# Performance work log

Hardware: AMD Instinct MI355X
Metric: run time of the kernel (lower is better)

## Reference

```python
import jax, jax.numpy as jnp
import numpy as np

H = 1024          # hidden_dim
N_AVAIL = 32768   # number of available ops (rows of the score matrix)
N_M = 64          # machines
N_OP = 40000      # unfinished ops
N_JOB = 2000      # jobs
L = 4             # policy_num_layers


def setup_inputs() -> dict:
    key = jax.random.key(0)
    ks = jax.random.split(key, 12)
    s_in = (2.0 / (2 * H + 2)) ** 0.5   # kaiming-ish scale
    s_h = (2.0 / H) ** 0.5
    return {
        "x_m": jax.random.normal(ks[0], (N_M, H), jnp.float32),
        "x_op": jax.random.normal(ks[1], (N_OP, H), jnp.float32),
        "job_srpt": jax.random.uniform(ks[2], (N_JOB,), jnp.float32),
        "pt": jax.random.uniform(ks[3], (N_AVAIL,), jnp.float32),  # process_time / max_process_time
        "W0": jax.random.normal(ks[4], (2 * H + 2, H), jnp.float32) * s_in,
        "b0": jnp.zeros((H,), jnp.float32),
        "W1": jax.random.normal(ks[5], (H, H), jnp.float32) * s_h,
        "b1": jnp.zeros((H,), jnp.float32),
        "W2": jax.random.normal(ks[6], (H, H), jnp.float32) * s_h,
        "b2": jnp.zeros((H,), jnp.float32),
        "W3": jax.random.normal(ks[7], (H, 1), jnp.float32) * s_h,
        "b3": jnp.zeros((1,), jnp.float32),
        "m_ids": jax.random.randint(ks[8], (N_AVAIL,), 0, N_M, jnp.int32),
        "op_idx": jax.random.randint(ks[9], (N_AVAIL,), 0, N_OP, jnp.int32),
        "job_ids": jax.random.randint(ks[10], (N_AVAIL,), 0, N_JOB, jnp.int32),
    }


def reference(x_m, x_op, job_srpt, pt, W0, b0, W1, b1, W2, b2, W3, b3,
              m_ids, op_idx, job_ids):
    # Batched gather + concat: replaces the per-op Python loop of torch.cat's.
    feat = jnp.concatenate(
        [x_m[m_ids],                     # [N, H]
         x_op[op_idx],                   # [N, H]
         job_srpt[job_ids][:, None],     # [N, 1]
         pt[:, None]],                   # [N, 1]
        axis=1)                          # [N, 2H+2]
    lrelu = lambda v: jax.nn.leaky_relu(v, 0.01)
    h = lrelu(feat @ W0 + b0)
    h = lrelu(h @ W1 + b1)
    h = lrelu(h @ W2 + b2)
    score = (h @ W3 + b3).ravel()        # [N]
    probs = jax.nn.softmax(score)        # softmax over available ops (dim=0)
    idx = jnp.argmax(score)              # greedy action
    return probs, idx
```

## Files before the change

kernel.cpp:

```cpp
#include <hip/hip_runtime.h>
#include <hip/hip_bf16.h>

typedef __attribute__((ext_vector_type(8))) short short8;
typedef __attribute__((ext_vector_type(4))) float f32x4;

#define GL2LDS16(g, l)                                                         \
  __builtin_amdgcn_global_load_lds(                                            \
      (const __attribute__((address_space(1))) unsigned int*)(g),              \
      (__attribute__((address_space(3))) unsigned int*)(l), 16, 0, 0)

__device__ __forceinline__ short8 lds_read_b128(const __hip_bfloat16* p) {
  short8 v;
  asm volatile("ds_read_b128 %0, %1"
               : "=v"(v)
               : "v"((unsigned)(uintptr_t)p));
  return v;
}

__global__ __launch_bounds__(256) void feat_kernel(
    const float* __restrict__ x_m, const float* __restrict__ x_op,
    const float* __restrict__ job_srpt, const int* __restrict__ m_ids,
    const int* __restrict__ op_idx, const int* __restrict__ job_ids,
    __hip_bfloat16* __restrict__ feat, float* __restrict__ srow) {
  const int row = blockIdx.x;
  const int t = threadIdx.x;
  const int j0 = t * 8;
  const float* src;
  if (j0 < 1024)
    src = x_m + (long)m_ids[row] * 1024 + j0;
  else
    src = x_op + (long)op_idx[row] * 1024 + (j0 - 1024);
  float4 v0 = *(const float4*)src;
  float4 v1 = *(const float4*)(src + 4);
  union {
    __hip_bfloat16 h[8];
    int4 i4;
  } u;
  u.h[0] = __float2bfloat16(v0.x);
  u.h[1] = __float2bfloat16(v0.y);
  u.h[2] = __float2bfloat16(v0.z);
  u.h[3] = __float2bfloat16(v0.w);
  u.h[4] = __float2bfloat16(v1.x);
  u.h[5] = __float2bfloat16(v1.y);
  u.h[6] = __float2bfloat16(v1.z);
  u.h[7] = __float2bfloat16(v1.w);
  *(int4*)&feat[(long)row * 2048 + j0] = u.i4;
  if (t == 0) srow[row] = job_srpt[job_ids[row]];
}

__global__ __launch_bounds__(256) void wconv_kernel(
    const float* __restrict__ W, __hip_bfloat16* __restrict__ Wt, int K) {
  __shared__ float tile[64][65];
  const int kb = blockIdx.x * 64;
  const int nb = blockIdx.y * 64;
  const int t = threadIdx.x;
#pragma unroll
  for (int it = 0; it < 16; ++it) {
    int idx = it * 256 + t;
    int kk = idx >> 6, nn = idx & 63;
    tile[kk][nn] = W[(long)(kb + kk) * 1024 + nb + nn];
  }
  __syncthreads();
#pragma unroll
  for (int it = 0; it < 16; ++it) {
    int idx = it * 256 + t;
    int nn = idx >> 6, kk = idx & 63;
    Wt[(long)(nb + nn) * K + kb + kk] = __float2bfloat16(tile[kk][nn]);
  }
}

__global__ __launch_bounds__(512, 2) void gemm_kernel(
    const __hip_bfloat16* __restrict__ A, const __hip_bfloat16* __restrict__ Bt,
    __hip_bfloat16* __restrict__ C, const float* __restrict__ bias, int M,
    int N, int K, int rank2, const float* __restrict__ wr0,
    const float* __restrict__ wr1, const float* __restrict__ srow,
    const float* __restrict__ ptv, int fuseW3,
    const float* __restrict__ W3, float* __restrict__ scoreOut) {
  __shared__ __align__(16) __hip_bfloat16 As[2][256 * 64];
  __shared__ __align__(16) __hip_bfloat16 Bs[2][256 * 64];
  const int t = threadIdx.x;
  const int lane = t & 63;
  const int wid = t >> 6;
  const int wm = wid >> 2;
  const int wn = wid & 3;
  const long arow0 = (long)blockIdx.x * 256;
  const int bcol0 = blockIdx.y * 256;
  const int NT = K >> 6;

  const int sa_row = ((t >> 8) * 128) + ((t >> 3) & 31);
  const int sb_row = t >> 3;
  const int scol = ((t & 7) ^ ((t >> 3) & 7)) * 8;

#define STAGE_A(buf, kt1, p)                                                   \
  GL2LDS16(A + (arow0 + sa_row + (p) * 32) * (long)K + (kt1) * 64 + scol,      \
           &As[buf][(t >> 8) * 8192 + (p) * 2048 + (t & 255) * 8])
#define STAGE_B(buf, kt1, q)                                                   \
  GL2LDS16(Bt + (long)(bcol0 + sb_row + (q) * 64) * (long)K + (kt1) * 64 + scol, \
           &Bs[buf][(q) * 4096 + t * 8])

  f32x4 acc[8][4] = {};
  short8 bfr[8];

#pragma unroll
  for (int q = 0; q < 4; ++q) STAGE_B(0, 0, q);
#pragma unroll
  for (int p = 0; p < 4; ++p) STAGE_A(0, 0, p);

  for (int kt = 0; kt < NT; ++kt) {
    const int cur = kt & 1;
    const bool pre = (kt + 1) < NT;
#pragma unroll
    for (int p = 0; p < 4; ++p) {
      if (pre) {
        if (p == 0) { STAGE_B(cur ^ 1, kt + 1, 0); STAGE_B(cur ^ 1, kt + 1, 1); }
        if (p == 1) { STAGE_B(cur ^ 1, kt + 1, 2); STAGE_B(cur ^ 1, kt + 1, 3); }
        if (p == 2) { STAGE_A(cur ^ 1, kt + 1, 0); STAGE_A(cur ^ 1, kt + 1, 1); }
        if (p == 3) { STAGE_A(cur ^ 1, kt + 1, 2); STAGE_A(cur ^ 1, kt + 1, 3); }
        asm volatile("s_waitcnt vmcnt(4)" ::: "memory");
      } else {
        asm volatile("s_waitcnt vmcnt(0)" ::: "memory");
      }
      __builtin_amdgcn_s_barrier();

      short8 af[2][2];
      if (p == 0) {
#pragma unroll
        for (int j = 0; j < 4; ++j)
#pragma unroll
          for (int ks = 0; ks < 2; ++ks) {
            const int ko = (ks * 32 + ((lane >> 4) << 3)) ^ ((lane & 7) << 3);
            bfr[j * 2 + ks] =
                lds_read_b128(&Bs[cur][(wn * 64 + j * 16 + (lane & 15)) * 64 + ko]);
          }
      }
#pragma unroll
      for (int ii = 0; ii < 2; ++ii)
#pragma unroll
        for (int ks = 0; ks < 2; ++ks) {
          const int ko = (ks * 32 + ((lane >> 4) << 3)) ^ ((lane & 7) << 3);
          af[ii][ks] = lds_read_b128(
              &As[cur][(wm * 128 + (2 * p + ii) * 16 + (lane & 15)) * 64 + ko]);
        }

      asm volatile("s_waitcnt lgkmcnt(0)" ::: "memory");
      __builtin_amdgcn_sched_barrier(0);
      __builtin_amdgcn_s_setprio(1);
#pragma unroll
      for (int ii = 0; ii < 2; ++ii)
#pragma unroll
        for (int ks = 0; ks < 2; ++ks)
#pragma unroll
          for (int j = 0; j < 4; ++j)
            acc[2 * p + ii][j] = __builtin_amdgcn_mfma_f32_16x16x32_bf16(
                af[ii][ks], bfr[j * 2 + ks], acc[2 * p + ii][j], 0, 0, 0);
      __builtin_amdgcn_s_setprio(0);
      __builtin_amdgcn_s_barrier();
    }
  }

  if (!fuseW3) {
#pragma unroll
    for (int j = 0; j < 4; ++j) {
      const int c = bcol0 + wn * 64 + j * 16 + (lane & 15);
      const float bia = bias[c];
      float wa = 0.f, wb = 0.f;
      if (rank2) {
        wa = wr0[c];
        wb = wr1[c];
      }
#pragma unroll
      for (int i = 0; i < 8; ++i) {
        const long rb = arow0 + wm * 128 + i * 16 + ((lane >> 4) << 2);
#pragma unroll
        for (int g = 0; g < 4; ++g) {
          const long r = rb + g;
          float v = acc[i][j][g] + bia;
          if (rank2) v += srow[r] * wa + ptv[r] * wb;
          v = v > 0.f ? v : 0.01f * v;
          C[r * N + c] = __float2bfloat16(v);
        }
      }
    }
  } else {
    float bia[4], w3v[4];
#pragma unroll
    for (int j = 0; j < 4; ++j) {
      const int c = bcol0 + wn * 64 + j * 16 + (lane & 15);
      bia[j] = bias[c];
      w3v[j] = W3[c];
    }
#pragma unroll
    for (int i = 0; i < 8; ++i) {
#pragma unroll
      for (int g = 0; g < 4; ++g) {
        float ps = 0.f;
#pragma unroll
        for (int j = 0; j < 4; ++j) {
          float v = acc[i][j][g] + bia[j];
          v = v > 0.f ? v : 0.01f * v;
          ps += v * w3v[j];
        }
        ps += __shfl_xor(ps, 1);
        ps += __shfl_xor(ps, 2);
        ps += __shfl_xor(ps, 4);
        ps += __shfl_xor(ps, 8);
        if ((lane & 15) == 0) {
          const long r = arow0 + wm * 128 + i * 16 + ((lane >> 4) << 2) + g;
          atomicAdd(&scoreOut[r], ps);
        }
      }
    }
  }
#undef STAGE_A
#undef STAGE_B
}

__global__ __launch_bounds__(256) void redmax_kernel(
    const float* __restrict__ score, float* __restrict__ pmax,
    int* __restrict__ pidx) {
  const int t = threadIdx.x, b = blockIdx.x;
  float m = -1e30f;
  int mi = 0;
#pragma unroll
  for (int u = 0; u < 2; ++u) {
    int i = b * 512 + u * 256 + t;
    float v = score[i];
    if (v > m) {
      m = v;
      mi = i;
    }
  }
  __shared__ float sm[4];
  __shared__ int si[4];
#pragma unroll
  for (int off = 32; off; off >>= 1) {
    float om = __shfl_down(m, off);
    int oi = __shfl_down(mi, off);
    if (om > m || (om == m && oi < mi)) {
      m = om;
      mi = oi;
    }
  }
  const int lane = t & 63, w = t >> 6;
  if (lane == 0) {
    sm[w] = m;
    si[w] = mi;
  }
  __syncthreads();
  if (t == 0) {
    for (int w2 = 1; w2 < 4; ++w2)
      if (sm[w2] > m || (sm[w2] == m && si[w2] < mi)) {
        m = sm[w2];
        mi = si[w2];
      }
    pmax[b] = m;
    pidx[b] = mi;
  }
}

__global__ __launch_bounds__(64) void finmax_kernel(
    const float* __restrict__ pmax, const int* __restrict__ pidx,
    float* __restrict__ gscal, float* __restrict__ out_idx) {
  const int t = threadIdx.x;
  float m = pmax[t];
  int mi = pidx[t];
#pragma unroll
  for (int off = 32; off; off >>= 1) {
    float om = __shfl_down(m, off);
    int oi = __shfl_down(mi, off);
    if (om > m || (om == m && oi < mi)) {
      m = om;
      mi = oi;
    }
  }
  if (t == 0) {
    gscal[0] = m;
    out_idx[0] = (float)mi;
  }
}

__global__ __launch_bounds__(256) void expsum_kernel(
    const float* __restrict__ score, const float* __restrict__ gscal,
    float* __restrict__ e, float* __restrict__ psum) {
  const int t = threadIdx.x, b = blockIdx.x;
  const float gmax = gscal[0];
  float s = 0.f;
#pragma unroll
  for (int u = 0; u < 2; ++u) {
    int i = b * 512 + u * 256 + t;
    float v = expf(score[i] - gmax);
    e[i] = v;
    s += v;
  }
#pragma unroll
  for (int off = 32; off; off >>= 1) s += __shfl_down(s, off);
  __shared__ float sm[4];
  const int lane = t & 63, w = t >> 6;
  if (lane == 0) sm[w] = s;
  __syncthreads();
  if (t == 0) psum[b] = sm[0] + sm[1] + sm[2] + sm[3];
}

__global__ __launch_bounds__(64) void finsum_kernel(const float* __restrict__ psum,
                                                    float* __restrict__ gscal) {
  float s = psum[threadIdx.x];
#pragma unroll
  for (int off = 32; off; off >>= 1) s += __shfl_down(s, off);
  if (threadIdx.x == 0) gscal[1] = 1.0f / s;
}

__global__ __launch_bounds__(256) void scale_kernel(float* __restrict__ e,
                                                    const float* __restrict__ gscal) {
  const float inv = gscal[1];
  const int i = blockIdx.x * 512 + threadIdx.x;
  e[i] *= inv;
  e[i + 256] *= inv;
}

extern "C" void kernel_launch(void* const* d_in, const int* in_sizes, int n_in,
                              void* d_out, int out_size, void* d_ws,
                              size_t ws_size, hipStream_t stream) {
  const float* x_m = (const float*)d_in[0];
  const float* x_op = (const float*)d_in[1];
  const float* job_srpt = (const float*)d_in[2];
  const float* pt = (const float*)d_in[3];
  const float* W0 = (const float*)d_in[4];
  const float* b0 = (const float*)d_in[5];
  const float* W1 = (const float*)d_in[6];
  const float* b1 = (const float*)d_in[7];
  const float* W2 = (const float*)d_in[8];
  const float* b2 = (const float*)d_in[9];
  const float* W3 = (const float*)d_in[10];
  const int* m_ids = (const int*)d_in[12];
  const int* op_idx = (const int*)d_in[13];
  const int* job_ids = (const int*)d_in[14];

  const int M = 32768;

  char* p = (char*)d_ws;
  __hip_bfloat16* feat = (__hip_bfloat16*)p;            p += (size_t)M * 2048 * 2;
  __hip_bfloat16* hA = (__hip_bfloat16*)p;              p += (size_t)M * 1024 * 2;
  __hip_bfloat16* hB = (__hip_bfloat16*)p;              p += (size_t)M * 1024 * 2;
  __hip_bfloat16* Wt0 = (__hip_bfloat16*)p;             p += (size_t)1024 * 2048 * 2;
  __hip_bfloat16* Wt1 = (__hip_bfloat16*)p;             p += (size_t)1024 * 1024 * 2;
  __hip_bfloat16* Wt2 = (__hip_bfloat16*)p;             p += (size_t)1024 * 1024 * 2;
  float* srow = (float*)p;                              p += (size_t)M * 4;
  float* score = (float*)p;                             p += (size_t)M * 4;
  float* pmax = (float*)p;                              p += 256;
  int* pidx = (int*)p;                                  p += 256;
  float* psum = (float*)p;                              p += 256;
  float* gscal = (float*)p;                             p += 256;

  float* probs = (float*)d_out;
  float* out_idx = probs + M;

  feat_kernel<<<M, 256, 0, stream>>>(x_m, x_op, job_srpt, m_ids, op_idx,
                                     job_ids, feat, srow);
  wconv_kernel<<<dim3(32, 16), 256, 0, stream>>>(W0, Wt0, 2048);
  wconv_kernel<<<dim3(16, 16), 256, 0, stream>>>(W1, Wt1, 1024);
  wconv_kernel<<<dim3(16, 16), 256, 0, stream>>>(W2, Wt2, 1024);
  hipMemsetAsync(score, 0, (size_t)M * 4, stream);

  gemm_kernel<<<dim3(128, 4), 512, 0, stream>>>(
      feat, Wt0, hA, b0, M, 1024, 2048, 1, W0 + (size_t)2048 * 1024,
      W0 + (size_t)2049 * 1024, srow, pt, 0, nullptr, nullptr);
  gemm_kernel<<<dim3(128, 4), 512, 0, stream>>>(hA, Wt1, hB, b1, M, 1024, 1024,
                                                0, nullptr, nullptr, nullptr,
                                                nullptr, 0, nullptr, nullptr);
  gemm_kernel<<<dim3(128, 4), 512, 0, stream>>>(hB, Wt2, nullptr, b2, M, 1024,
                                                1024, 0, nullptr, nullptr,
                                                nullptr, nullptr, 1, W3, score);

  redmax_kernel<<<64, 256, 0, stream>>>(score, pmax, pidx);
  finmax_kernel<<<1, 64, 0, stream>>>(pmax, pidx, gscal, out_idx);
  expsum_kernel<<<64, 256, 0, stream>>>(score, gscal, probs, psum);
  finsum_kernel<<<1, 64, 0, stream>>>(psum, gscal);
  scale_kernel<<<64, 256, 0, stream>>>(probs, gscal);
}
```

Measured before the change: 409.9 us.

## Precompute x_m @ W0 table for 64 machines and halve first GEMM K

Because x_m has only 64 distinct rows, the product x_m @ W0[:1024] is computed once into a 64x1024 fp32 table by a small kernel. The first GEMM now only multiplies the gathered x_op features (K=1024 instead of 2048), and its epilogue adds the table row selected by m_ids. This removes half of the layer-0 MFMA work and halves the gathered feature buffer, at the cost of a scattered fp32 table lookup per output element in the epilogue and a naive fp32 table kernel. The machine part is now computed in fp32 instead of bf16.

After: 448.0 us. 9.3% more time.

```diff
diff --git a/kernel.cpp b/kernel.cpp
--- a/kernel.cpp
+++ b/kernel.cpp
@@ -17,19 +17,13 @@
   return v;
 }
 
-__global__ __launch_bounds__(256) void feat_kernel(
-    const float* __restrict__ x_m, const float* __restrict__ x_op,
-    const float* __restrict__ job_srpt, const int* __restrict__ m_ids,
+__global__ __launch_bounds__(256) void featB_kernel(
+    const float* __restrict__ x_op, const float* __restrict__ job_srpt,
     const int* __restrict__ op_idx, const int* __restrict__ job_ids,
-    __hip_bfloat16* __restrict__ feat, float* __restrict__ srow) {
-  const int row = blockIdx.x;
-  const int t = threadIdx.x;
-  const int j0 = t * 8;
-  const float* src;
-  if (j0 < 1024)
-    src = x_m + (long)m_ids[row] * 1024 + j0;
-  else
-    src = x_op + (long)op_idx[row] * 1024 + (j0 - 1024);
+    __hip_bfloat16* __restrict__ featB, float* __restrict__ srow) {
+  const long row = (long)blockIdx.x * 2 + (threadIdx.x >> 7);
+  const int t = threadIdx.x & 127;
+  const float* src = x_op + (long)op_idx[row] * 1024 + t * 8;
   float4 v0 = *(const float4*)src;
   float4 v1 = *(const float4*)(src + 4);
   union {
@@ -44,8 +38,20 @@
   u.h[5] = __float2bfloat16(v1.y);
   u.h[6] = __float2bfloat16(v1.z);
   u.h[7] = __float2bfloat16(v1.w);
-  *(int4*)&feat[(long)row * 2048 + j0] = u.i4;
+  *(int4*)&featB[row * 1024 + t * 8] = u.i4;
   if (t == 0) srow[row] = job_srpt[job_ids[row]];
+}
+
+__global__ __launch_bounds__(256) void pm_kernel(const float* __restrict__ x_m,
+                                                 const float* __restrict__ W0,
+                                                 float* __restrict__ P_m) {
+  const int c = blockIdx.x * 256 + threadIdx.x;
+  const int m = blockIdx.y;
+  const float* xr = x_m + m * 1024;
+  float s = 0.f;
+#pragma unroll 4
+  for (int k = 0; k < 1024; ++k) s += xr[k] * W0[(long)k * 1024 + c];
+  P_m[m * 1024 + c] = s;
 }
 
 __global__ __launch_bounds__(256) void wconv_kernel(
@@ -75,7 +81,8 @@
     int N, int K, int rank2, const float* __restrict__ wr0,
     const float* __restrict__ wr1, const float* __restrict__ srow,
     const float* __restrict__ ptv, int fuseW3,
-    const float* __restrict__ W3, float* __restrict__ scoreOut) {
+    const float* __restrict__ W3, float* __restrict__ scoreOut,
+    const float* __restrict__ pmTab, const int* __restrict__ mids) {
   __shared__ __align__(16) __hip_bfloat16 As[2][256 * 64];
   __shared__ __align__(16) __hip_bfloat16 Bs[2][256 * 64];
   const int t = threadIdx.x;
@@ -159,23 +166,31 @@
   }
 
   if (!fuseW3) {
+    float bia[4], wa[4], wb[4];
 #pragma unroll
     for (int j = 0; j < 4; ++j) {
       const int c = bcol0 + wn * 64 + j * 16 + (lane & 15);
-      const float bia = bias[c];
-      float wa = 0.f, wb = 0.f;
-      if (rank2) {
-        wa = wr0[c];
-        wb = wr1[c];
-      }
-#pragma unroll
-      for (int i = 0; i < 8; ++i) {
-        const long rb = arow0 + wm * 128 + i * 16 + ((lane >> 4) << 2);
-#pragma unroll
-        for (int g = 0; g < 4; ++g) {
-          const long r = rb + g;
-          float v = acc[i][j][g] + bia;
-          if (rank2) v += srow[r] * wa + ptv[r] * wb;
+      bia[j] = bias[c];
+      wa[j] = rank2 ? wr0[c] : 0.f;
+      wb[j] = rank2 ? wr1[c] : 0.f;
+    }
+#pragma unroll
+    for (int i = 0; i < 8; ++i) {
+#pragma unroll
+      for (int g = 0; g < 4; ++g) {
+        const long r = arow0 + wm * 128 + i * 16 + ((lane >> 4) << 2) + g;
+        float sr = 0.f, pv = 0.f;
+        if (rank2) {
+          sr = srow[r];
+          pv = ptv[r];
+        }
+        const float* pmrow = pmTab ? (pmTab + (long)mids[r] * 1024) : nullptr;
+#pragma unroll
+        for (int j = 0; j < 4; ++j) {
+          const int c = bcol0 + wn * 64 + j * 16 + (lane & 15);
+          float v = acc[i][j][g] + bia[j];
+          if (rank2) v += sr * wa[j] + pv * wb[j];
+          if (pmrow) v += pmrow[c];
           v = v > 0.f ? v : 0.01f * v;
           C[r * N + c] = __float2bfloat16(v);
         }
@@ -338,12 +353,13 @@
   const int M = 32768;
 
   char* p = (char*)d_ws;
-  __hip_bfloat16* feat = (__hip_bfloat16*)p;            p += (size_t)M * 2048 * 2;
+  __hip_bfloat16* featB = (__hip_bfloat16*)p;           p += (size_t)M * 1024 * 2;
   __hip_bfloat16* hA = (__hip_bfloat16*)p;              p += (size_t)M * 1024 * 2;
   __hip_bfloat16* hB = (__hip_bfloat16*)p;              p += (size_t)M * 1024 * 2;
-  __hip_bfloat16* Wt0 = (__hip_bfloat16*)p;             p += (size_t)1024 * 2048 * 2;
+  __hip_bfloat16* Wt0b = (__hip_bfloat16*)p;            p += (size_t)1024 * 1024 * 2;
   __hip_bfloat16* Wt1 = (__hip_bfloat16*)p;             p += (size_t)1024 * 1024 * 2;
   __hip_bfloat16* Wt2 = (__hip_bfloat16*)p;             p += (size_t)1024 * 1024 * 2;
+  float* P_m = (float*)p;                               p += (size_t)64 * 1024 * 4;
   float* srow = (float*)p;                              p += (size_t)M * 4;
   float* score = (float*)p;                             p += (size_t)M * 4;
   float* pmax = (float*)p;                              p += 256;
@@ -354,22 +370,24 @@
   float* probs = (float*)d_out;
   float* out_idx = probs + M;
 
-  feat_kernel<<<M, 256, 0, stream>>>(x_m, x_op, job_srpt, m_ids, op_idx,
-                                     job_ids, feat, srow);
-  wconv_kernel<<<dim3(32, 16), 256, 0, stream>>>(W0, Wt0, 2048);
+  featB_kernel<<<M / 2, 256, 0, stream>>>(x_op, job_srpt, op_idx, job_ids,
+                                          featB, srow);
+  pm_kernel<<<dim3(4, 64), 256, 0, stream>>>(x_m, W0, P_m);
+  wconv_kernel<<<dim3(16, 16), 256, 0, stream>>>(W0 + (size_t)1024 * 1024, Wt0b,
+                                                 1024);
   wconv_kernel<<<dim3(16, 16), 256, 0, stream>>>(W1, Wt1, 1024);
   wconv_kernel<<<dim3(16, 16), 256, 0, stream>>>(W2, Wt2, 1024);
   hipMemsetAsync(score, 0, (size_t)M * 4, stream);
 
   gemm_kernel<<<dim3(128, 4), 512, 0, stream>>>(
-      feat, Wt0, hA, b0, M, 1024, 2048, 1, W0 + (size_t)2048 * 1024,
-      W0 + (size_t)2049 * 1024, srow, pt, 0, nullptr, nullptr);
-  gemm_kernel<<<dim3(128, 4), 512, 0, stream>>>(hA, Wt1, hB, b1, M, 1024, 1024,
-                                                0, nullptr, nullptr, nullptr,
-                                                nullptr, 0, nullptr, nullptr);
-  gemm_kernel<<<dim3(128, 4), 512, 0, stream>>>(hB, Wt2, nullptr, b2, M, 1024,
-                                                1024, 0, nullptr, nullptr,
-                                                nullptr, nullptr, 1, W3, score);
+      featB, Wt0b, hA, b0, M, 1024, 1024, 1, W0 + (size_t)2048 * 1024,
+      W0 + (size_t)2049 * 1024, srow, pt, 0, nullptr, nullptr, P_m, m_ids);
+  gemm_kernel<<<dim3(128, 4), 512, 0, stream>>>(
+      hA, Wt1, hB, b1, M, 1024, 1024, 0, nullptr, nullptr, nullptr, nullptr, 0,
+      nullptr, nullptr, nullptr, nullptr);
+  gemm_kernel<<<dim3(128, 4), 512, 0, stream>>>(
+      hB, Wt2, nullptr, b2, M, 1024, 1024, 0, nullptr, nullptr, nullptr,
+      nullptr, 1, W3, score, nullptr, nullptr);
 
   redmax_kernel<<<64, 256, 0, stream>>>(score, pmax, pidx);
   finmax_kernel<<<1, 64, 0, stream>>>(pmax, pidx, gscal, out_idx);
```
